# Optimization experiments

Hardware: AMD Instinct MI355X
Metric: run time of the kernel (lower is better)

The kernel has to match this reference:

```python
import jax, jax.numpy as jnp
import numpy as np

GROUPS = 32
EPS = 1e-6


def group_norm(x, gamma, beta):
    b, c, h, w = x.shape
    xg = x.reshape(b, GROUPS, c // GROUPS, h, w)
    mean = xg.mean(axis=(2, 3, 4), keepdims=True)
    var = xg.var(axis=(2, 3, 4), keepdims=True)
    xn = (xg - mean) * jax.lax.rsqrt(var + EPS)
    xn = xn.reshape(b, c, h, w)
    return xn * gamma[None, :, None, None] + beta[None, :, None, None]


def conv1x1(x, w, b):
    # x: [B,C,H,W], w: [O,C], b: [O]
    return jnp.einsum('bchw,oc->bohw', x, w) + b[None, :, None, None]


def setup_inputs() -> dict:
    key = jax.random.key(0)
    ks = jax.random.split(key, 6)
    C = 512
    B, H, W = 2, 64, 64
    s = (C) ** -0.5  # fan-in style init scale for 1x1 convs
    return {
        'x': jax.random.normal(ks[0], (B, C, H, W), jnp.float32),
        'gn_gamma': jnp.ones((C,), jnp.float32),
        'gn_beta': jnp.zeros((C,), jnp.float32),
        'wq': jax.random.normal(ks[1], (C, C), jnp.float32) * s,
        'bq': jnp.zeros((C,), jnp.float32),
        'wk': jax.random.normal(ks[2], (C, C), jnp.float32) * s,
        'bk': jnp.zeros((C,), jnp.float32),
        'wv': jax.random.normal(ks[3], (C, C), jnp.float32) * s,
        'bv': jnp.zeros((C,), jnp.float32),
        'wo': jax.random.normal(ks[4], (C, C), jnp.float32) * s,
        'bo': jnp.zeros((C,), jnp.float32),
    }


def reference(x, gn_gamma, gn_beta, wq, bq, wk, bk, wv, bv, wo, bo):
    b, c, h, w = x.shape
    n = h * w
    h_ = group_norm(x, gn_gamma, gn_beta)
    q = conv1x1(h_, wq, bq).reshape(b, c, n)   # [B,C,N]
    k = conv1x1(h_, wk, bk).reshape(b, c, n)   # [B,C,N]
    v = conv1x1(h_, wv, bv).reshape(b, c, n)   # [B,C,N]
    scale = jnp.asarray(int(c) ** (-0.5), x.dtype)
    # scores[b, nq, nk] = sum_c q[b,c,nq] * k[b,c,nk]
    scores = jnp.einsum('bcn,bcm->bnm', q, k) * scale
    attn = jax.nn.softmax(scores, axis=2)      # softmax over keys
    # out[b,c,nq] = sum_m v[b,c,m] * attn[b,nq,m]
    out = jnp.einsum('bcm,bnm->bcn', v, attn).reshape(b, c, h, w)
    out = conv1x1(out, wo, bo)
    return x + out
```

## Files before the change

kernel.cpp:

```cpp
#include <hip/hip_runtime.h>

typedef unsigned short u16;
typedef __attribute__((ext_vector_type(8))) unsigned short ushort8;
typedef __attribute__((ext_vector_type(8))) short bf16x8;
typedef __attribute__((ext_vector_type(4))) float f32x4;

#define DEVINL __device__ __forceinline__

DEVINL float bf2f(u16 u){ union{unsigned i; float f;} v; v.i = ((unsigned)u) << 16; return v.f; }
DEVINL u16 f2bf(float f){
  unsigned x = __builtin_bit_cast(unsigned, f);
  x += 0x7fffu + ((x >> 16) & 1u);
  return (u16)(x >> 16);
}
DEVINL void gl_lds16(const void* g, void* l){
  __builtin_amdgcn_global_load_lds((const __attribute__((address_space(1))) unsigned*)g,
                                   (__attribute__((address_space(3))) unsigned*)l, 16, 0, 0);
}
template<int N> DEVINL void wait_vmcnt(){
  asm volatile("s_waitcnt vmcnt(%0)" :: "n"(N) : "memory");
}
DEVINL void hard_barrier(){
  asm volatile("" ::: "memory");
  __builtin_amdgcn_s_barrier();
  asm volatile("" ::: "memory");
}
DEVINL float wsum(float v){
  #pragma unroll
  for (int o = 32; o; o >>= 1) v += __shfl_xor(v, o, 64);
  return v;
}

__global__ __launch_bounds__(256) void cvt4b_k(const float* __restrict__ s0, const float* __restrict__ s1,
                 const float* __restrict__ s2, const float* __restrict__ s3,
                 const float* __restrict__ bq, const float* __restrict__ bk, const float* __restrict__ bv,
                 u16* __restrict__ wdst, float* __restrict__ bdst){
  if (blockIdx.x == 512){
    for (int j = threadIdx.x; j < 1536; j += 256)
      bdst[j] = (j < 512) ? bq[j] : (j < 1024) ? bk[j-512] : bv[j-1024];
    return;
  }
  const int g = blockIdx.x >> 7;
  const float* src = (g==0) ? s0 : (g==1) ? s1 : (g==2) ? s2 : s3;
  const int i = ((blockIdx.x & 127)*256 + threadIdx.x)*8;
  float4 f0 = *(const float4*)(src + i);
  float4 f1 = *(const float4*)(src + i + 4);
  ushort8 o;
  o[0]=f2bf(f0.x); o[1]=f2bf(f0.y); o[2]=f2bf(f0.z); o[3]=f2bf(f0.w);
  o[4]=f2bf(f1.x); o[5]=f2bf(f1.y); o[6]=f2bf(f1.z); o[7]=f2bf(f1.w);
  *(ushort8*)(wdst + g*262144 + i) = o;
}

__global__ __launch_bounds__(256) void rowinv_k(const float* __restrict__ psum, float* __restrict__ inv){
  const int row = blockIdx.x*256 + threadIdx.x;
  float s = 0.f;
  #pragma unroll 8
  for (int sl = 0; sl < 64; ++sl) s += psum[sl*8192 + row];
  inv[row] = 1.f / s;
}

__global__ __launch_bounds__(256) void reduce4_k(const u16* __restrict__ part,
                 const float* __restrict__ inv, u16* __restrict__ dst){
  const int i = (blockIdx.x*256 + threadIdx.x)*8;
  const u16* p = part + (size_t)blockIdx.y*8388608;
  float a[8] = {};
  #pragma unroll
  for (int ks = 0; ks < 4; ++ks){
    ushort8 u = *(const ushort8*)(p + (size_t)ks*2097152 + i);
    #pragma unroll
    for (int j = 0; j < 8; ++j) a[j] += bf2f(u[j]);
  }
  const float iv = inv[blockIdx.y*4096 + (i >> 9)];
  ushort8 o;
  #pragma unroll
  for (int j = 0; j < 8; ++j) o[j] = f2bf(a[j] * iv);
  *(ushort8*)(dst + (size_t)blockIdx.y*2097152 + i) = o;
}

__global__ __launch_bounds__(256) void gn_stats_k(const float* __restrict__ x, float* __restrict__ stats){
  __shared__ __align__(16) float red[8];
  const float* px = x + ((size_t)blockIdx.x << 16);
  const int t = threadIdx.x;
  float s = 0.f, ss = 0.f;
  for (int off = t*4; off < 65536; off += 1024){
    float4 u = *(const float4*)(px + off);
    s  += u.x + u.y + u.z + u.w;
    ss += u.x*u.x + u.y*u.y + u.z*u.z + u.w*u.w;
  }
  s = wsum(s); ss = wsum(ss);
  if ((t & 63) == 0){ red[t>>6] = s; red[4+(t>>6)] = ss; }
  __syncthreads();
  if (t == 0){
    float S1 = red[0]+red[1]+red[2]+red[3];
    float S2 = red[4]+red[5]+red[6]+red[7];
    float mean = S1 * (1.f/65536.f);
    float var  = S2 * (1.f/65536.f) - mean*mean;
    stats[2*blockIdx.x]   = mean;
    stats[2*blockIdx.x+1] = rsqrtf(var + 1e-6f);
  }
}

__global__ __launch_bounds__(256) void gn_apply_k(const float* __restrict__ x, const float* __restrict__ gamma,
                 const float* __restrict__ beta, const float* __restrict__ stats, u16* __restrict__ ht){
  __shared__ __align__(16) u16 tile[32*512];
  const int b = blockIdx.y, n0 = blockIdx.x*32, t = threadIdx.x;
  #pragma unroll
  for (int it = 0; it < 8; ++it){
    int c  = it*64 + (t>>2);
    int nn = (t&3)*8;
    const float* px = x + ((size_t)(b*512 + c) << 12) + n0 + nn;
    float4 u0 = *(const float4*)(px);
    float4 u1 = *(const float4*)(px + 4);
    float mean = stats[2*(b*32 + (c>>4))];
    float rstd = stats[2*(b*32 + (c>>4)) + 1];
    float ga = gamma[c], be = beta[c];
    float f[8] = {u0.x,u0.y,u0.z,u0.w,u1.x,u1.y,u1.z,u1.w};
    #pragma unroll
    for (int j = 0; j < 8; ++j)
      tile[(nn+j)*512 + c] = f2bf((f[j] - mean) * rstd * ga + be);
  }
  __syncthreads();
  const int rw = t>>3, sg = t&7;
  #pragma unroll
  for (int uu = 0; uu < 8; ++uu){
    ushort8 v = *(const ushort8*)(tile + rw*512 + sg*64 + uu*8);
    *(ushort8*)(ht + ((size_t)(b*4096 + n0 + rw) << 9) + sg*64 + uu*8) = v;
  }
}

template<bool EXPSUM>
__global__ __launch_bounds__(512) void gemm8_nt(
    const u16* __restrict__ A, const u16* __restrict__ Bt, u16* __restrict__ C,
    float* __restrict__ psum,
    int K, int lda, int ldb, int ldc, int zdiv,
    long long aStrB, long long aStr, long long bStrB, long long bStr,
    long long cStrB, long long cStr)
{
  extern __shared__ __align__(16) char smem[];
  const int z = blockIdx.z, z1 = z / zdiv, z2 = z % zdiv;
  A  += (size_t)aStrB*z1 + (size_t)aStr*z2;
  Bt += (size_t)bStrB*z1 + (size_t)bStr*z2;
  C  += (size_t)cStrB*z1 + (size_t)cStr*z2;
  const int nwg = gridDim.x*gridDim.y;
  int wg = blockIdx.y*gridDim.x + blockIdx.x;
  wg = (wg & 7)*(nwg >> 3) + (wg >> 3);
  const int m0 = (wg / gridDim.x)*256, n0 = (wg % gridDim.x)*256;

  const int t = threadIdx.x, wv = t>>6, ln = t&63;
  const int wm = wv>>2, wn = wv&3;
  const int lq = ln&15, lg = ln>>4;
  const int srow = ln>>2;
  const int sseg = (((ln&3) ^ ((srow>>1)&3)))*8;
  const int rslot = (lg ^ ((lq>>1)&3))*16;

  auto STAGE_A = [&](int d, int kh, int kkn){
    char* base = smem + d*32768 + kh*16384 + wv*1024;
    const u16* g = A + (size_t)(m0 + wv*16 + srow)*lda + kkn + kh*32 + sseg;
    gl_lds16(g, base);
    gl_lds16(g + (size_t)128*lda, base + 8192);
  };
  auto STAGE_B = [&](int d, int kh, int kkn){
    char* base = smem + 65536 + d*32768 + kh*16384 + wv*1024;
    const u16* g = Bt + (size_t)(n0 + wv*16 + srow)*ldb + kkn + kh*32 + sseg;
    gl_lds16(g, base);
    gl_lds16(g + (size_t)128*ldb, base + 8192);
  };
  auto LDA4 = [&](int d, int ks, int mh, bf16x8* a){
    const char* p = smem + d*32768 + ks*16384 + (wm*128 + mh*64 + lq)*64 + rslot;
    #pragma unroll
    for (int i = 0; i < 4; ++i) a[i] = *(const bf16x8*)(p + i*1024);
  };
  auto LDB4 = [&](int d, int ks, bf16x8* b){
    const char* p = smem + 65536 + d*32768 + ks*16384 + (wn*64 + lq)*64 + rslot;
    #pragma unroll
    for (int j = 0; j < 4; ++j) b[j] = *(const bf16x8*)(p + j*1024);
  };

  f32x4 acc[8][4] = {};
  auto MFMA16 = [&](bf16x8* a4, bf16x8* b4, int moff){
    __builtin_amdgcn_s_setprio(1);
    #pragma unroll
    for (int n = 0; n < 4; ++n)
      #pragma unroll
      for (int m = 0; m < 4; ++m)
        acc[moff+m][n] = __builtin_amdgcn_mfma_f32_16x16x32_bf16(a4[m], b4[n], acc[moff+m][n], 0, 0, 0);
    __builtin_amdgcn_s_setprio(0);
  };

  STAGE_A(0,0,0); STAGE_B(0,0,0); STAGE_A(0,1,0); STAGE_B(0,1,0);
  wait_vmcnt<4>();
  hard_barrier();
  const int T = K >> 6;
  int d = 0;
  for (int tt = 0; tt < T; ++tt){
    const int kkn = (tt+1) << 6;
    const bool st = (tt + 1 < T);
    bf16x8 a[4], b[4];
    LDA4(d, 0, 0, a); LDB4(d, 0, b);
    if (st) STAGE_A(d^1, 0, kkn);
    hard_barrier();
    MFMA16(a, b, 0);
    hard_barrier();
    LDA4(d, 0, 1, a);
    if (st) STAGE_B(d^1, 0, kkn);
    if (st) wait_vmcnt<4>(); else wait_vmcnt<0>();
    hard_barrier();
    MFMA16(a, b, 4);
    hard_barrier();
    LDA4(d, 1, 0, a); LDB4(d, 1, b);
    if (st) STAGE_A(d^1, 1, kkn);
    hard_barrier();
    MFMA16(a, b, 0);
    hard_barrier();
    LDA4(d, 1, 1, a);
    if (st) STAGE_B(d^1, 1, kkn);
    if (st) wait_vmcnt<4>(); else wait_vmcnt<0>();
    hard_barrier();
    MFMA16(a, b, 4);
    hard_barrier();
    d ^= 1;
  }
  const int slice = EXPSUM ? ((n0 >> 8)*4 + wn) : 0;
  #pragma unroll
  for (int m = 0; m < 8; ++m)
    #pragma unroll
    for (int r2 = 0; r2 < 4; ++r2){
      const int mg = m0 + wm*128 + m*16 + lg*4 + r2;
      u16* cp = C + (size_t)mg*ldc + n0 + wn*64 + lq;
      if constexpr (EXPSUM){
        float e[4], rs = 0.f;
        #pragma unroll
        for (int n = 0; n < 4; ++n){ e[n] = __expf(acc[m][n][r2]); rs += e[n]; }
        rs += __shfl_xor(rs, 1, 64);
        rs += __shfl_xor(rs, 2, 64);
        rs += __shfl_xor(rs, 4, 64);
        rs += __shfl_xor(rs, 8, 64);
        if (lq == 0) psum[slice*8192 + z1*4096 + mg] = rs;
        #pragma unroll
        for (int n = 0; n < 4; ++n) cp[n*16] = f2bf(e[n]);
      } else {
        #pragma unroll
        for (int n = 0; n < 4; ++n) cp[n*16] = f2bf(acc[m][n][r2]);
      }
    }
}

__global__ __launch_bounds__(256) void qkv_k(
    const u16* __restrict__ Wstk, const u16* __restrict__ ht,
    const float* __restrict__ biases, u16* __restrict__ dstBase)
{
  __shared__ __align__(16) char smem[32768];
  char* smA0 = smem;
  char* smA1 = smem + 8192;
  char* smB0 = smem + 16384;
  char* smB1 = smem + 24576;
  const int z = blockIdx.z, mat = z >> 1, b = z & 1;
  const u16* A  = Wstk + mat*262144;
  const u16* Bt = ht + (size_t)b*2097152;
  const float* bias = biases + mat*512;
  const float oscale = (mat == 0) ? 0.044194173824159216f : 1.0f;
  u16* dst = dstBase + (size_t)mat*4194304 + (size_t)b*2097152;
  const int m0 = blockIdx.y*128, n0 = blockIdx.x*128;
  const int t = threadIdx.x, wv = t>>6, ln = t&63;
  const int wm = wv>>1, wn = wv&1;
  const int lq = ln&15, lg = ln>>4;
  const int srow = ln>>2;
  const int sseg = (((ln&3) ^ ((srow>>1)&3)))*8;
  const int rslot = (lg ^ ((lq>>1)&3))*16;
  f32x4 acc[4][4] = {};
  for (int kk = 0; kk < 512; kk += 64){
    __syncthreads();
    #pragma unroll
    for (int r = 0; r < 2; ++r){
      const int rr = r*64 + wv*16;
      const u16* pa = A  + (size_t)(m0 + rr + srow)*512 + kk + sseg;
      const u16* pb = Bt + (size_t)(n0 + rr + srow)*512 + kk + sseg;
      gl_lds16(pa,      smA0 + rr*64);
      gl_lds16(pa + 32, smA1 + rr*64);
      gl_lds16(pb,      smB0 + rr*64);
      gl_lds16(pb + 32, smB1 + rr*64);
    }
    __syncthreads();
    #pragma unroll
    for (int half = 0; half < 2; ++half){
      const char* pA = half ? smA1 : smA0;
      const char* pB = half ? smB1 : smB0;
      bf16x8 af[4], bfv[4];
      #pragma unroll
      for (int i = 0; i < 4; ++i) af[i]  = *(const bf16x8*)(pA + ((wm*64 + i*16 + lq)<<6) + rslot);
      #pragma unroll
      for (int j = 0; j < 4; ++j) bfv[j] = *(const bf16x8*)(pB + ((wn*64 + j*16 + lq)<<6) + rslot);
      #pragma unroll
      for (int i = 0; i < 4; ++i)
        #pragma unroll
        for (int j = 0; j < 4; ++j)
          acc[i][j] = __builtin_amdgcn_mfma_f32_16x16x32_bf16(af[i], bfv[j], acc[i][j], 0, 0, 0);
    }
  }
  if (mat == 2){
    #pragma unroll
    for (int i = 0; i < 4; ++i)
      #pragma unroll
      for (int r2 = 0; r2 < 4; ++r2){
        const int mg = m0 + wm*64 + i*16 + lg*4 + r2;
        float bv = bias[mg];
        #pragma unroll
        for (int j = 0; j < 4; ++j){
          const int ng = n0 + wn*64 + j*16 + lq;
          dst[(size_t)mg*4096 + ng] = f2bf(acc[i][j][r2] + bv);
        }
      }
  } else {
    __syncthreads();
    u16* ct = (u16*)smem;
    #pragma unroll
    for (int i = 0; i < 4; ++i)
      #pragma unroll
      for (int j = 0; j < 4; ++j)
        #pragma unroll
        for (int r2 = 0; r2 < 4; ++r2){
          const int ml = wm*64 + i*16 + lg*4 + r2;
          const int nl = wn*64 + j*16 + lq;
          ct[nl*128 + ml] = f2bf((acc[i][j][r2] + bias[m0 + ml]) * oscale);
        }
    __syncthreads();
    const int rw = t>>1, hf = (t&1)*64;
    #pragma unroll
    for (int u = 0; u < 8; ++u){
      *(ushort8*)(dst + (size_t)(n0 + rw)*512 + m0 + hf + u*8) =
          *(const ushort8*)(ct + rw*128 + hf + u*8);
    }
  }
}

template<bool TRANS_OUT, bool HAS_BIAS, bool HAS_RES, bool F32OUT>
__global__ __launch_bounds__(256) void gemm_nt(
    const u16* __restrict__ A, const u16* __restrict__ Bt,
    const float* __restrict__ bias, const float* __restrict__ res, void* __restrict__ Cw_,
    int K, int lda, int ldb, int ldc, int zdiv,
    long long aStrB, long long aStr, long long bStrB, long long bStr,
    long long cStrB, long long cStr, long long rStrB, float oscale)
{
  __shared__ __align__(16) char smem[32768];
  char* smA0 = smem;
  char* smA1 = smem + 8192;
  char* smB0 = smem + 16384;
  char* smB1 = smem + 24576;
  const int z = blockIdx.z;
  const int z1 = z / zdiv, z2 = z % zdiv;
  A  += (size_t)aStrB*z1 + (size_t)aStr*z2;
  Bt += (size_t)bStrB*z1 + (size_t)bStr*z2;
  u16*   Cw16 = (u16*)Cw_   + (size_t)cStrB*z1 + (size_t)cStr*z2;
  float* Cw32 = (float*)Cw_ + (size_t)cStrB*z1 + (size_t)cStr*z2;
  const float* resp = HAS_RES ? (res + (size_t)rStrB*z1) : nullptr;
  const int m0 = blockIdx.y*128, n0 = blockIdx.x*128;
  const int t = threadIdx.x, wv = t>>6, ln = t&63;
  const int wm = wv>>1, wn = wv&1;
  const int lq = ln&15, lg = ln>>4;
  const int srow = ln>>2;
  const int sseg = (((ln&3) ^ ((srow>>1)&3)))*8;
  const int rslot = (lg ^ ((lq>>1)&3))*16;
  f32x4 acc[4][4] = {};
  for (int kk = 0; kk < K; kk += 64){
    __syncthreads();
    #pragma unroll
    for (int r = 0; r < 2; ++r){
      const int rr = r*64 + wv*16;
      const u16* pa = A  + (size_t)(m0 + rr + srow)*lda + kk + sseg;
      const u16* pb = Bt + (size_t)(n0 + rr + srow)*ldb + kk + sseg;
      gl_lds16(pa,      smA0 + rr*64);
      gl_lds16(pa + 32, smA1 + rr*64);
      gl_lds16(pb,      smB0 + rr*64);
      gl_lds16(pb + 32, smB1 + rr*64);
    }
    __syncthreads();
    #pragma unroll
    for (int half = 0; half < 2; ++half){
      const char* pA = half ? smA1 : smA0;
      const char* pB = half ? smB1 : smB0;
      bf16x8 af[4], bfv[4];
      #pragma unroll
      for (int i = 0; i < 4; ++i) af[i]  = *(const bf16x8*)(pA + ((wm*64 + i*16 + lq)<<6) + rslot);
      #pragma unroll
      for (int j = 0; j < 4; ++j) bfv[j] = *(const bf16x8*)(pB + ((wn*64 + j*16 + lq)<<6) + rslot);
      #pragma unroll
      for (int i = 0; i < 4; ++i)
        #pragma unroll
        for (int j = 0; j < 4; ++j)
          acc[i][j] = __builtin_amdgcn_mfma_f32_16x16x32_bf16(af[i], bfv[j], acc[i][j], 0, 0, 0);
    }
  }
  if constexpr (!TRANS_OUT){
    #pragma unroll
    for (int i = 0; i < 4; ++i){
      #pragma unroll
      for (int r2 = 0; r2 < 4; ++r2){
        const int mg = m0 + wm*64 + i*16 + lg*4 + r2;
        float bv = HAS_BIAS ? bias[mg] : 0.f;
        #pragma unroll
        for (int j = 0; j < 4; ++j){
          const int ng = n0 + wn*64 + j*16 + lq;
          float v = (acc[i][j][r2] + bv) * oscale;
          if (HAS_RES) v += resp[(size_t)mg*ldc + ng];
          if constexpr (F32OUT) Cw32[(size_t)mg*ldc + ng] = v;
          else                  Cw16[(size_t)mg*ldc + ng] = f2bf(v);
        }
      }
    }
  } else {
    __syncthreads();
    u16* ct = (u16*)smem;
    #pragma unroll
    for (int i = 0; i < 4; ++i)
      #pragma unroll
      for (int j = 0; j < 4; ++j)
        #pragma unroll
        for (int r2 = 0; r2 < 4; ++r2){
          const int ml = wm*64 + i*16 + lg*4 + r2;
          const int nl = wn*64 + j*16 + lq;
          float v = acc[i][j][r2];
          if (HAS_BIAS) v += bias[m0 + ml];
          ct[nl*128 + ml] = f2bf(v * oscale);
        }
    __syncthreads();
    const int rw = t>>1, hf = (t&1)*64;
    #pragma unroll
    for (int u = 0; u < 8; ++u){
      *(ushort8*)(Cw16 + (size_t)(n0 + rw)*ldc + m0 + hf + u*8) =
          *(const ushort8*)(ct + rw*128 + hf + u*8);
    }
  }
}

extern "C" void kernel_launch(void* const* d_in, const int* in_sizes, int n_in,
                              void* d_out, int out_size, void* d_ws, size_t ws_size,
                              hipStream_t stream)
{
  const float* x   = (const float*)d_in[0];
  const float* gam = (const float*)d_in[1];
  const float* bet = (const float*)d_in[2];
  const float* wq  = (const float*)d_in[3];
  const float* bq  = (const float*)d_in[4];
  const float* wk  = (const float*)d_in[5];
  const float* bk  = (const float*)d_in[6];
  const float* wvp = (const float*)d_in[7];
  const float* bv  = (const float*)d_in[8];
  const float* wo  = (const float*)d_in[9];
  const float* bo  = (const float*)d_in[10];
  float* out = (float*)d_out;

  char* w = (char*)d_ws;
  float* stats   = (float*)w;
  float* psum    = (float*)(w + 4096);
  float* inv     = (float*)(w + 2101248);
  float* biasQKV = (float*)(w + 2134016);
  u16* wqb  = (u16*)(w + (size_t)4194304);
  u16* wob  = wqb + 3*262144;
  u16* Qt   = wqb + 4*262144;
  u16* Kt   = Qt + 4194304;
  u16* Vb   = Kt + 4194304;
  u16* attT = Vb + 4194304;
  u16* Sbuf = attT + 4194304;
  u16* part = Sbuf + 33554432;
  u16* ht   = (u16*)d_out;

  const long long NC = 4096LL*512, NN = 4096LL*4096;

  cvt4b_k<<<dim3(513), dim3(256), 0, stream>>>(wq, wk, wvp, wo, bq, bk, bv, wqb, biasQKV);
  gn_stats_k<<<dim3(64), dim3(256), 0, stream>>>(x, stats);
  gn_apply_k<<<dim3(128,2), dim3(256), 0, stream>>>(x, gam, bet, stats, ht);
  qkv_k<<<dim3(32,4,6), dim3(256), 0, stream>>>(wqb, ht, biasQKV, Qt);
  gemm8_nt<true><<<dim3(16,16,2), dim3(512), 131072, stream>>>(
      Qt, Kt, Sbuf, psum, 512, 512, 512, 4096, 1, NC, 0, NC, 0, NN, 0);
  rowinv_k<<<dim3(32), dim3(256), 0, stream>>>(psum, inv);
  gemm8_nt<false><<<dim3(2,16,8), dim3(512), 131072, stream>>>(
      Sbuf, Vb, part, nullptr, 1024, 4096, 4096, 512, 4,
      NN, 1024, NC, 1024, 8388608, 2097152);
  reduce4_k<<<dim3(1024,2), dim3(256), 0, stream>>>(part, inv, attT);
  gemm_nt<false, true, true, true><<<dim3(32,4,2), dim3(256), 0, stream>>>(
      wob, attT, bo, x, out, 512, 512, 512, 4096, 1, 0,0, NC,0, NC,0, NC, 1.0f);
}
```

Measured before the change: 188.6 us.

## Deepen GEMM LDS pipeline to four half-tile stages and fuse row-inverse into reduce

Measured after the change: 187.1 us. No clear change (-0.8%).

```diff
diff --git a/kernel.cpp b/kernel.cpp
--- a/kernel.cpp
+++ b/kernel.cpp
@@ -51,17 +51,16 @@
   *(ushort8*)(wdst + g*262144 + i) = o;
 }
 
-__global__ __launch_bounds__(256) void rowinv_k(const float* __restrict__ psum, float* __restrict__ inv){
-  const int row = blockIdx.x*256 + threadIdx.x;
-  float s = 0.f;
-  #pragma unroll 8
-  for (int sl = 0; sl < 64; ++sl) s += psum[sl*8192 + row];
-  inv[row] = 1.f / s;
-}
-
 __global__ __launch_bounds__(256) void reduce4_k(const u16* __restrict__ part,
-                 const float* __restrict__ inv, u16* __restrict__ dst){
-  const int i = (blockIdx.x*256 + threadIdx.x)*8;
+                 const float* __restrict__ psum, u16* __restrict__ dst){
+  __shared__ float invsh[4];
+  const int t = threadIdx.x, w = t>>6, ln = t&63;
+  const int row = blockIdx.x*4 + w;
+  float s = psum[ln*8192 + blockIdx.y*4096 + row];
+  s = wsum(s);
+  if (ln == 0) invsh[w] = 1.f / s;
+  __syncthreads();
+  const int i = (blockIdx.x*256 + t)*8;
   const u16* p = part + (size_t)blockIdx.y*8388608;
   float a[8] = {};
   #pragma unroll
@@ -70,7 +69,7 @@
     #pragma unroll
     for (int j = 0; j < 8; ++j) a[j] += bf2f(u[j]);
   }
-  const float iv = inv[blockIdx.y*4096 + (i >> 9)];
+  const float iv = invsh[w];
   ushort8 o;
   #pragma unroll
   for (int j = 0; j < 8; ++j) o[j] = f2bf(a[j] * iv);
@@ -153,25 +152,25 @@
   const int sseg = (((ln&3) ^ ((srow>>1)&3)))*8;
   const int rslot = (lg ^ ((lq>>1)&3))*16;
 
-  auto STAGE_A = [&](int d, int kh, int kkn){
-    char* base = smem + d*32768 + kh*16384 + wv*1024;
-    const u16* g = A + (size_t)(m0 + wv*16 + srow)*lda + kkn + kh*32 + sseg;
+  auto STAGE_A = [&](int u){
+    char* base = smem + (u&3)*16384 + wv*1024;
+    const u16* g = A + (size_t)(m0 + wv*16 + srow)*lda + u*32 + sseg;
     gl_lds16(g, base);
     gl_lds16(g + (size_t)128*lda, base + 8192);
   };
-  auto STAGE_B = [&](int d, int kh, int kkn){
-    char* base = smem + 65536 + d*32768 + kh*16384 + wv*1024;
-    const u16* g = Bt + (size_t)(n0 + wv*16 + srow)*ldb + kkn + kh*32 + sseg;
+  auto STAGE_B = [&](int u){
+    char* base = smem + 65536 + (u&3)*16384 + wv*1024;
+    const u16* g = Bt + (size_t)(n0 + wv*16 + srow)*ldb + u*32 + sseg;
     gl_lds16(g, base);
     gl_lds16(g + (size_t)128*ldb, base + 8192);
   };
-  auto LDA4 = [&](int d, int ks, int mh, bf16x8* a){
-    const char* p = smem + d*32768 + ks*16384 + (wm*128 + mh*64 + lq)*64 + rslot;
+  auto LDA4 = [&](int u, int mh, bf16x8* a){
+    const char* p = smem + (u&3)*16384 + (wm*128 + mh*64 + lq)*64 + rslot;
     #pragma unroll
     for (int i = 0; i < 4; ++i) a[i] = *(const bf16x8*)(p + i*1024);
   };
-  auto LDB4 = [&](int d, int ks, bf16x8* b){
-    const char* p = smem + 65536 + d*32768 + ks*16384 + (wn*64 + lq)*64 + rslot;
+  auto LDB4 = [&](int u, bf16x8* b){
+    const char* p = smem + 65536 + (u&3)*16384 + (wn*64 + lq)*64 + rslot;
     #pragma unroll
     for (int j = 0; j < 4; ++j) b[j] = *(const bf16x8*)(p + j*1024);
   };
@@ -187,38 +186,36 @@
     __builtin_amdgcn_s_setprio(0);
   };
 
-  STAGE_A(0,0,0); STAGE_B(0,0,0); STAGE_A(0,1,0); STAGE_B(0,1,0);
-  wait_vmcnt<4>();
+  STAGE_A(0); STAGE_B(0); STAGE_A(1); STAGE_B(1); STAGE_A(2); STAGE_B(2);
+  wait_vmcnt<8>();
   hard_barrier();
   const int T = K >> 6;
-  int d = 0;
   for (int tt = 0; tt < T; ++tt){
-    const int kkn = (tt+1) << 6;
-    const bool st = (tt + 1 < T);
+    const int u0 = 2*tt, u1 = 2*tt + 1;
     bf16x8 a[4], b[4];
-    LDA4(d, 0, 0, a); LDB4(d, 0, b);
-    if (st) STAGE_A(d^1, 0, kkn);
+    LDA4(u0, 0, a); LDB4(u0, b);
+    if (tt < T-1) STAGE_A(u0+3);
     hard_barrier();
     MFMA16(a, b, 0);
     hard_barrier();
-    LDA4(d, 0, 1, a);
-    if (st) STAGE_B(d^1, 0, kkn);
-    if (st) wait_vmcnt<4>(); else wait_vmcnt<0>();
+    LDA4(u0, 1, a);
+    if (tt < T-1) STAGE_B(u0+3);
+    if (tt == T-1) wait_vmcnt<0>(); else wait_vmcnt<8>();
     hard_barrier();
     MFMA16(a, b, 4);
     hard_barrier();
-    LDA4(d, 1, 0, a); LDB4(d, 1, b);
-    if (st) STAGE_A(d^1, 1, kkn);
+    LDA4(u1, 0, a); LDB4(u1, b);
+    if (tt < T-2) STAGE_A(u0+4);
     hard_barrier();
     MFMA16(a, b, 0);
     hard_barrier();
-    LDA4(d, 1, 1, a);
-    if (st) STAGE_B(d^1, 1, kkn);
-    if (st) wait_vmcnt<4>(); else wait_vmcnt<0>();
+    LDA4(u1, 1, a);
+    if (tt < T-2) STAGE_B(u0+4);
+    if (tt == T-2)      wait_vmcnt<4>();
+    else if (tt < T-2)  wait_vmcnt<8>();
     hard_barrier();
     MFMA16(a, b, 4);
     hard_barrier();
-    d ^= 1;
   }
   const int slice = EXPSUM ? ((n0 >> 8)*4 + wn) : 0;
   #pragma unroll
@@ -452,7 +449,6 @@
   char* w = (char*)d_ws;
   float* stats   = (float*)w;
   float* psum    = (float*)(w + 4096);
-  float* inv     = (float*)(w + 2101248);
   float* biasQKV = (float*)(w + 2134016);
   u16* wqb  = (u16*)(w + (size_t)4194304);
   u16* wob  = wqb + 3*262144;
@@ -472,11 +468,10 @@
   qkv_k<<<dim3(32,4,6), dim3(256), 0, stream>>>(wqb, ht, biasQKV, Qt);
   gemm8_nt<true><<<dim3(16,16,2), dim3(512), 131072, stream>>>(
       Qt, Kt, Sbuf, psum, 512, 512, 512, 4096, 1, NC, 0, NC, 0, NN, 0);
-  rowinv_k<<<dim3(32), dim3(256), 0, stream>>>(psum, inv);
   gemm8_nt<false><<<dim3(2,16,8), dim3(512), 131072, stream>>>(
       Sbuf, Vb, part, nullptr, 1024, 4096, 4096, 512, 4,
       NN, 1024, NC, 1024, 8388608, 2097152);
-  reduce4_k<<<dim3(1024,2), dim3(256), 0, stream>>>(part, inv, attT);
+  reduce4_k<<<dim3(1024,2), dim3(256), 0, stream>>>(part, psum, attT);
   gemm_nt<false, true, true, true><<<dim3(32,4,2), dim3(256), 0, stream>>>(
       wob, attT, bo, x, out, 512, 512, 512, 4096, 1, 0,0, NC,0, NC,0, NC, 1.0f);
 }
```
